# Optimization experiments

Hardware: AMD Instinct MI355X
Metric: run time of the kernel (lower is better)

Reference implementation:

```python
import jax, jax.numpy as jnp
import numpy as np

NEG_SLOPE = 0.2  # PyG GATConv default LeakyReLU slope


def gat_layer(x, src, dst, W, a_src, a_dst, bias, heads, out_dim, concat, n_nodes):
    # x: [N, F_in]; W: [F_in, heads*out_dim]
    h = (x @ W).reshape(n_nodes, heads, out_dim)          # [N, H, C]
    alpha_src = jnp.sum(h * a_src, axis=-1)               # [N, H]
    alpha_dst = jnp.sum(h * a_dst, axis=-1)               # [N, H]
    e = jax.nn.leaky_relu(alpha_src[src] + alpha_dst[dst], NEG_SLOPE)  # [E, H]
    # softmax over edges grouped by destination node (self-loops guarantee nonempty segments)
    m = jax.ops.segment_max(e, dst, num_segments=n_nodes)  # [N, H]
    w = jnp.exp(e - m[dst])
    s = jax.ops.segment_sum(w, dst, num_segments=n_nodes)  # [N, H]
    alpha = w / s[dst]                                     # [E, H]
    msg = h[src] * alpha[:, :, None]                       # [E, H, C]
    out = jax.ops.segment_sum(msg, dst, num_segments=n_nodes)  # [N, H, C]
    if concat:
        out = out.reshape(n_nodes, heads * out_dim)
    else:
        out = out.mean(axis=1)
    return out + bias


def setup_inputs() -> dict:
    key = jax.random.key(0)
    ks = jax.random.split(key, 12)
    N, E = 50000, 600000
    F_IN, OUT = 256, 64
    H1, C1 = 2, 2 * OUT          # conv1: heads=2, per-head dim 128
    F2 = H1 * C1                 # 256
    x = jax.random.normal(ks[0], (N, F_IN), dtype=jnp.float32)
    edge_index = jax.random.randint(ks[1], (2, E), 0, N, dtype=jnp.int64)
    g1 = 1.0 / np.sqrt(F_IN)
    g2 = 1.0 / np.sqrt(F2)
    return {
        "x": x,
        "edge_index": edge_index,
        "W1": jax.random.normal(ks[2], (F_IN, H1 * C1), dtype=jnp.float32) * g1,
        "a1_src": jax.random.normal(ks[3], (H1, C1), dtype=jnp.float32) * g2,
        "a1_dst": jax.random.normal(ks[4], (H1, C1), dtype=jnp.float32) * g2,
        "b1": jnp.zeros((H1 * C1,), dtype=jnp.float32),
        "W2": jax.random.normal(ks[5], (F2, OUT), dtype=jnp.float32) * g2,
        "a2_src": jax.random.normal(ks[6], (1, OUT), dtype=jnp.float32) * 0.1,
        "a2_dst": jax.random.normal(ks[7], (1, OUT), dtype=jnp.float32) * 0.1,
        "b2": jnp.zeros((OUT,), dtype=jnp.float32),
    }


def reference(x, edge_index, W1, a1_src, a1_dst, b1, W2, a2_src, a2_dst, b2):
    N = x.shape[0]
    # add self-loops (PyG GATConv default)
    loops = jnp.arange(N, dtype=edge_index.dtype)
    src = jnp.concatenate([edge_index[0], loops])
    dst = jnp.concatenate([edge_index[1], loops])
    OUT = W2.shape[1]
    h = gat_layer(x, src, dst, W1, a1_src, a1_dst, b1,
                  heads=2, out_dim=2 * OUT, concat=True, n_nodes=N)
    h = jax.nn.elu(h)
    out = gat_layer(h, src, dst, W2, a2_src, a2_dst, b2,
                    heads=1, out_dim=OUT, concat=False, n_nodes=N)
    return out
```

## Files before the change

### kernel.cpp

```cpp
#include <hip/hip_runtime.h>
#include <hip/hip_bf16.h>
#include <math.h>


#define NSLOPE 0.2f

using bf16x8 = __attribute__((ext_vector_type(8))) short;
using f32x4  = __attribute__((ext_vector_type(4))) float;
using u16x8  = __attribute__((ext_vector_type(8))) unsigned short;
using u16x4  = __attribute__((ext_vector_type(4))) unsigned short;

__device__ __forceinline__ unsigned short bf16_rne(float f) {
    unsigned u = __float_as_uint(f);
    return (unsigned short)((u + 0x7FFFu + ((u >> 16) & 1u)) >> 16);
}
__device__ __forceinline__ float bf16_to_f(unsigned short h) {
    return __uint_as_float(((unsigned)h) << 16);
}

__global__ __launch_bounds__(256) void k_prep_all(const float* __restrict__ x,
                                                  const float* __restrict__ W1,
                                                  const float* __restrict__ W2,
                                                  unsigned short* __restrict__ Xhi,
                                                  unsigned short* __restrict__ W1hi,
                                                  unsigned short* __restrict__ W2hi,
                                                  int* __restrict__ cnt,
                                                  int BX, int total4, int N) {
    int b = blockIdx.x, t = threadIdx.x;
    if (b < BX) {
        int id = b * 256 + t;
        if (id >= total4) return;
        float4 v = *(const float4*)&x[(size_t)id * 4];
        unsigned short hi[4];
        hi[0] = bf16_rne(v.x); hi[1] = bf16_rne(v.y);
        hi[2] = bf16_rne(v.z); hi[3] = bf16_rne(v.w);
        *(u16x4*)&Xhi[(size_t)id * 4] = *(u16x4*)hi;
    } else if (b < BX + 64) {
        int id = (b - BX) * 256 + t;
        int n = id >> 6, kg = id & 63;
        unsigned short hi[4];
#pragma unroll
        for (int c = 0; c < 4; ++c) {
            float w = W1[(kg * 4 + c) * 256 + n];
            hi[c] = bf16_rne(w);
        }
        *(u16x4*)&W1hi[n * 256 + kg * 4] = *(u16x4*)hi;
    } else if (b < BX + 128) {
        int id = (b - BX - 64) * 256 + t;
        int n = id >> 8, k = id & 255;
        W2hi[n * 256 + k] = bf16_rne(W2[k * 64 + n]);
    } else {
        int i = (b - BX - 128) * 256 + t;
        if (i < N) cnt[i] = 0;
    }
}

#define G1S 40
__global__ __launch_bounds__(256) void k_gemm1(const unsigned short* __restrict__ Xhi,
                                               const unsigned short* __restrict__ Whi,
                                               const float* __restrict__ a1s,
                                               const float* __restrict__ a1d,
                                               unsigned short* __restrict__ h1b,
                                               float* __restrict__ as_,
                                               float* __restrict__ ad_, int M,
                                               const int* __restrict__ esrc,
                                               const int* __restrict__ edst,
                                               int* __restrict__ cnt,
                                               int* __restrict__ bucket,
                                               int E, int G1B) {
    __shared__ unsigned short sAh[128 * G1S];
    __shared__ unsigned short sBh[256 * G1S];
    __shared__ float salS[128][2], salD[128][2];
    int t = threadIdx.x;
    if (blockIdx.x >= G1B) {
        int i = (blockIdx.x - G1B) * 256 + t;
        if (i < E) {
            int s = esrc[i], d = edst[i];
            int p = atomicAdd(&cnt[d], 1);
            if (p < 63) bucket[(size_t)d * 64 + p] = s;
        }
        return;
    }
    int lane = t & 63, wave = t >> 6;
    int q = lane >> 4, m = lane & 15;
    int row0 = blockIdx.x * 128;
    int rbase = (wave & 1) * 64;
    int head = wave >> 1;
    int cbase = head * 128;
    f32x4 acc[4][8];
#pragma unroll
    for (int i = 0; i < 4; ++i)
#pragma unroll
        for (int j = 0; j < 8; ++j) acc[i][j] = (f32x4){0.f, 0.f, 0.f, 0.f};

    for (int kc = 0; kc < 256; kc += 32) {
#pragma unroll
        for (int i2 = 0; i2 < 2; ++i2) {
            int slot = t + i2 * 256;
            int r = slot >> 2, kg = slot & 3;
            int row = row0 + r;
            u16x8 vh = {0, 0, 0, 0, 0, 0, 0, 0};
            if (row < M) vh = *(const u16x8*)&Xhi[(size_t)row * 256 + kc + kg * 8];
            *(u16x8*)&sAh[r * G1S + kg * 8] = vh;
        }
#pragma unroll
        for (int i2 = 0; i2 < 4; ++i2) {
            int slot = t + i2 * 256;
            int n = slot >> 2, kg = slot & 3;
            *(u16x8*)&sBh[n * G1S + kg * 8] =
                *(const u16x8*)&Whi[(size_t)n * 256 + kc + kg * 8];
        }
        __syncthreads();
        bf16x8 ah[4], bh[8];
#pragma unroll
        for (int i = 0; i < 4; ++i)
            ah[i] = *(bf16x8*)&sAh[(rbase + i * 16 + m) * G1S + q * 8];
#pragma unroll
        for (int j = 0; j < 8; ++j)
            bh[j] = *(bf16x8*)&sBh[(cbase + j * 16 + m) * G1S + q * 8];
#pragma unroll
        for (int i = 0; i < 4; ++i)
#pragma unroll
            for (int j = 0; j < 8; ++j)
                acc[i][j] = __builtin_amdgcn_mfma_f32_16x16x32_bf16(ah[i], bh[j], acc[i][j], 0, 0, 0);
        __syncthreads();
    }
    float sv[8], dv[8];
#pragma unroll
    for (int j = 0; j < 8; ++j) {
        sv[j] = a1s[cbase + j * 16 + m];
        dv[j] = a1d[cbase + j * 16 + m];
    }
#pragma unroll
    for (int i = 0; i < 4; ++i) {
#pragma unroll
        for (int r = 0; r < 4; ++r) {
            int rl = rbase + i * 16 + q * 4 + r;
            int row = row0 + rl;
            float ps = 0.f, pd = 0.f;
#pragma unroll
            for (int j = 0; j < 8; ++j) {
                ps += acc[i][j][r] * sv[j];
                pd += acc[i][j][r] * dv[j];
            }
#pragma unroll
            for (int mask = 1; mask < 16; mask <<= 1) {
                ps += __shfl_xor(ps, mask, 64);
                pd += __shfl_xor(pd, mask, 64);
            }
            if (m == 0) {
                salS[rl][head] = ps;
                salD[rl][head] = pd;
            }
            if (row < M) {
#pragma unroll
                for (int j = 0; j < 8; ++j)
                    h1b[(size_t)row * 256 + cbase + j * 16 + m] = bf16_rne(acc[i][j][r]);
            }
        }
    }
    __syncthreads();
    if (t < 128) {
        int row = row0 + t;
        if (row < M) {
            as_[row * 2 + 0] = salS[t][0];
            as_[row * 2 + 1] = salS[t][1];
            ad_[row * 2 + 0] = salD[t][0];
            ad_[row * 2 + 1] = salD[t][1];
        }
    }
}

__global__ __launch_bounds__(256) void k_agg1(const unsigned short* __restrict__ h1b,
                                              const float* __restrict__ as,
                                              const float* __restrict__ ad,
                                              const int* __restrict__ cnt,
                                              const int* __restrict__ bucket,
                                              const float* __restrict__ b1,
                                              unsigned short* __restrict__ helu_b, int N) {
    int wid = (blockIdx.x * blockDim.x + threadIdx.x) >> 6;
    int lane = threadIdx.x & 63;
    if (wid >= N) return;
    int c = min(cnt[wid], 63);
    int cntTot = c + 1;
    float ad0 = ad[wid * 2], ad1 = ad[wid * 2 + 1];
    int half = lane >> 5, hl = lane & 31;
    int headL = hl >> 4;
    float acc[8];
#pragma unroll
    for (int cc = 0; cc < 8; ++cc) acc[cc] = 0.f;
    float sumw = 0.f;

    int s = (lane < c) ? bucket[(size_t)wid * 64 + lane] : wid;
    float w0 = 0.f, w1 = 0.f;
    if (lane <= c) {
        float2 av = *(const float2*)&as[s * 2];
        float l0 = av.x + ad0; l0 = l0 >= 0.f ? l0 : NSLOPE * l0;
        float l1 = av.y + ad1; l1 = l1 >= 0.f ? l1 : NSLOPE * l1;
        w0 = __expf(l0); w1 = __expf(l1);
    }
    int pairs = (cntTot + 1) >> 1;
    int jj = 0;
    for (; jj + 4 <= pairs; jj += 4) {
        int e0 = 2 * jj + half, e1 = e0 + 2, e2 = e0 + 4, e3 = e0 + 6;
        int sa = __shfl(s, e0, 64), sb = __shfl(s, e1, 64);
        int sc = __shfl(s, e2, 64), se = __shfl(s, e3, 64);
        float wa0 = __shfl(w0, e0, 64), wa1 = __shfl(w1, e0, 64);
        float wb0 = __shfl(w0, e1, 64), wb1 = __shfl(w1, e1, 64);
        float wc0 = __shfl(w0, e2, 64), wc1 = __shfl(w1, e2, 64);
        float wd0 = __shfl(w0, e3, 64), wd1 = __shfl(w1, e3, 64);
        u16x8 hva = *(const u16x8*)&h1b[(size_t)sa * 256 + hl * 8];
        u16x8 hvb = *(const u16x8*)&h1b[(size_t)sb * 256 + hl * 8];
        u16x8 hvc = *(const u16x8*)&h1b[(size_t)sc * 256 + hl * 8];
        u16x8 hvd = *(const u16x8*)&h1b[(size_t)se * 256 + hl * 8];
        float wa = headL ? wa1 : wa0;
        float wb = headL ? wb1 : wb0;
        float wc = headL ? wc1 : wc0;
        float wd = headL ? wd1 : wd0;
        sumw += (wa + wb) + (wc + wd);
#pragma unroll
        for (int cc = 0; cc < 8; ++cc)
            acc[cc] += (wa * bf16_to_f(hva[cc]) + wb * bf16_to_f(hvb[cc]))
                     + (wc * bf16_to_f(hvc[cc]) + wd * bf16_to_f(hvd[cc]));
    }
    for (; jj + 2 <= pairs; jj += 2) {
        int e0 = 2 * jj + half, e1 = e0 + 2;
        int sa = __shfl(s, e0, 64), sb = __shfl(s, e1, 64);
        float wa0 = __shfl(w0, e0, 64), wa1 = __shfl(w1, e0, 64);
        float wb0 = __shfl(w0, e1, 64), wb1 = __shfl(w1, e1, 64);
        u16x8 hva = *(const u16x8*)&h1b[(size_t)sa * 256 + hl * 8];
        u16x8 hvb = *(const u16x8*)&h1b[(size_t)sb * 256 + hl * 8];
        float wa = headL ? wa1 : wa0;
        float wb = headL ? wb1 : wb0;
        sumw += wa + wb;
#pragma unroll
        for (int cc = 0; cc < 8; ++cc)
            acc[cc] += wa * bf16_to_f(hva[cc]) + wb * bf16_to_f(hvb[cc]);
    }
    for (; jj < pairs; ++jj) {
        int e0 = 2 * jj + half;
        int sa = __shfl(s, e0, 64);
        float wa0 = __shfl(w0, e0, 64), wa1 = __shfl(w1, e0, 64);
        u16x8 hva = *(const u16x8*)&h1b[(size_t)sa * 256 + hl * 8];
        float wa = headL ? wa1 : wa0;
        sumw += wa;
#pragma unroll
        for (int cc = 0; cc < 8; ++cc) acc[cc] += wa * bf16_to_f(hva[cc]);
    }
#pragma unroll
    for (int cc = 0; cc < 8; ++cc) acc[cc] += __shfl_xor(acc[cc], 32, 64);
    sumw += __shfl_xor(sumw, 32, 64);
    float inv = 1.0f / sumw;
    int ch = hl * 8 + half * 4;
    float4 bv = *(const float4*)&b1[ch];
    float bb[4] = {bv.x, bv.y, bv.z, bv.w};
    unsigned short o[4];
#pragma unroll
    for (int cc = 0; cc < 4; ++cc) {
        float v = acc[half * 4 + cc] * inv + bb[cc];
        v = v > 0.f ? v : expm1f(v);
        o[cc] = bf16_rne(v);
    }
    *(u16x4*)&helu_b[(size_t)wid * 256 + ch] = *(u16x4*)o;
}

__global__ __launch_bounds__(256) void k_gemm2(const unsigned short* __restrict__ hb,
                                               const unsigned short* __restrict__ Whi,
                                               const float* __restrict__ a2s,
                                               const float* __restrict__ a2d,
                                               unsigned short* __restrict__ h2b,
                                               float* __restrict__ as_,
                                               float* __restrict__ ad_, int M) {
    __shared__ unsigned short sA[128 * G1S];
    __shared__ unsigned short sBh[64 * G1S];
    int t = threadIdx.x;
    int lane = t & 63, wave = t >> 6;
    int q = lane >> 4, m = lane & 15;
    int row0 = blockIdx.x * 128;
    int rbase = wave * 32;
    f32x4 acc[2][4];
#pragma unroll
    for (int i = 0; i < 2; ++i)
#pragma unroll
        for (int j = 0; j < 4; ++j) acc[i][j] = (f32x4){0.f, 0.f, 0.f, 0.f};

    for (int kc = 0; kc < 256; kc += 32) {
#pragma unroll
        for (int i = 0; i < 2; ++i) {
            int slot = t + i * 256;
            int r = slot >> 2, kg = slot & 3;
            int row = row0 + r;
            u16x8 v = {0, 0, 0, 0, 0, 0, 0, 0};
            if (row < M) v = *(const u16x8*)&hb[(size_t)row * 256 + kc + kg * 8];
            *(u16x8*)&sA[r * G1S + kg * 8] = v;
        }
        {
            int n = t >> 2, kg = t & 3;
            *(u16x8*)&sBh[n * G1S + kg * 8] =
                *(const u16x8*)&Whi[(size_t)n * 256 + kc + kg * 8];
        }
        __syncthreads();
        bf16x8 a[2], bh[4];
#pragma unroll
        for (int i = 0; i < 2; ++i)
            a[i] = *(bf16x8*)&sA[(rbase + i * 16 + m) * G1S + q * 8];
#pragma unroll
        for (int j = 0; j < 4; ++j)
            bh[j] = *(bf16x8*)&sBh[(j * 16 + m) * G1S + q * 8];
#pragma unroll
        for (int i = 0; i < 2; ++i)
#pragma unroll
            for (int j = 0; j < 4; ++j)
                acc[i][j] = __builtin_amdgcn_mfma_f32_16x16x32_bf16(a[i], bh[j], acc[i][j], 0, 0, 0);
        __syncthreads();
    }
    float sv[4], dv[4];
#pragma unroll
    for (int j = 0; j < 4; ++j) {
        sv[j] = a2s[j * 16 + m];
        dv[j] = a2d[j * 16 + m];
    }
#pragma unroll
    for (int i = 0; i < 2; ++i) {
#pragma unroll
        for (int r = 0; r < 4; ++r) {
            int row = row0 + rbase + i * 16 + q * 4 + r;
            float ps = acc[i][0][r] * sv[0] + acc[i][1][r] * sv[1]
                     + acc[i][2][r] * sv[2] + acc[i][3][r] * sv[3];
            float pd = acc[i][0][r] * dv[0] + acc[i][1][r] * dv[1]
                     + acc[i][2][r] * dv[2] + acc[i][3][r] * dv[3];
#pragma unroll
            for (int mask = 1; mask < 16; mask <<= 1) {
                ps += __shfl_xor(ps, mask, 64);
                pd += __shfl_xor(pd, mask, 64);
            }
            if (row < M) {
#pragma unroll
                for (int j = 0; j < 4; ++j)
                    h2b[(size_t)row * 64 + j * 16 + m] = bf16_rne(acc[i][j][r]);
                if (m == 0) { as_[row] = ps; ad_[row] = pd; }
            }
        }
    }
}

__global__ __launch_bounds__(256) void k_agg2(const unsigned short* __restrict__ h2b,
                                              const float* __restrict__ as,
                                              const float* __restrict__ ad,
                                              const int* __restrict__ cnt,
                                              const int* __restrict__ bucket,
                                              const float* __restrict__ b2,
                                              float* __restrict__ out, int N) {
    int wid = (blockIdx.x * blockDim.x + threadIdx.x) >> 6;
    int lane = threadIdx.x & 63;
    if (wid >= N) return;
    int c = min(cnt[wid], 63);
    int cntTot = c + 1;
    float adw = ad[wid];
    int g = lane >> 4, gl = lane & 15;
    float acc[4];
#pragma unroll
    for (int cc = 0; cc < 4; ++cc) acc[cc] = 0.f;
    float sumw = 0.f;

    int s = (lane < c) ? bucket[(size_t)wid * 64 + lane] : wid;
    float w = 0.f;
    if (lane <= c) {
        float l = as[s] + adw;
        l = l >= 0.f ? l : NSLOPE * l;
        w = __expf(l);
    }
    int quads = (cntTot + 3) >> 2;
    int jj = 0;
    for (; jj + 4 <= quads; jj += 4) {
        int e0 = 4 * jj + g, e1 = e0 + 4, e2 = e0 + 8, e3 = e0 + 12;
        int sa = __shfl(s, e0, 64), sb = __shfl(s, e1, 64);
        int sc = __shfl(s, e2, 64), se = __shfl(s, e3, 64);
        float wa = __shfl(w, e0, 64), wb = __shfl(w, e1, 64);
        float wc = __shfl(w, e2, 64), wd = __shfl(w, e3, 64);
        u16x4 hva = *(const u16x4*)&h2b[(size_t)sa * 64 + gl * 4];
        u16x4 hvb = *(const u16x4*)&h2b[(size_t)sb * 64 + gl * 4];
        u16x4 hvc = *(const u16x4*)&h2b[(size_t)sc * 64 + gl * 4];
        u16x4 hvd = *(const u16x4*)&h2b[(size_t)se * 64 + gl * 4];
        sumw += (wa + wb) + (wc + wd);
        acc[0] += (wa * bf16_to_f(hva.x) + wb * bf16_to_f(hvb.x))
                + (wc * bf16_to_f(hvc.x) + wd * bf16_to_f(hvd.x));
        acc[1] += (wa * bf16_to_f(hva.y) + wb * bf16_to_f(hvb.y))
                + (wc * bf16_to_f(hvc.y) + wd * bf16_to_f(hvd.y));
        acc[2] += (wa * bf16_to_f(hva.z) + wb * bf16_to_f(hvb.z))
                + (wc * bf16_to_f(hvc.z) + wd * bf16_to_f(hvd.z));
        acc[3] += (wa * bf16_to_f(hva.w) + wb * bf16_to_f(hvb.w))
                + (wc * bf16_to_f(hvc.w) + wd * bf16_to_f(hvd.w));
    }
    for (; jj + 2 <= quads; jj += 2) {
        int e0 = 4 * jj + g, e1 = e0 + 4;
        int sa = __shfl(s, e0, 64), sb = __shfl(s, e1, 64);
        float wa = __shfl(w, e0, 64), wb = __shfl(w, e1, 64);
        u16x4 hva = *(const u16x4*)&h2b[(size_t)sa * 64 + gl * 4];
        u16x4 hvb = *(const u16x4*)&h2b[(size_t)sb * 64 + gl * 4];
        sumw += wa + wb;
        acc[0] += wa * bf16_to_f(hva.x) + wb * bf16_to_f(hvb.x);
        acc[1] += wa * bf16_to_f(hva.y) + wb * bf16_to_f(hvb.y);
        acc[2] += wa * bf16_to_f(hva.z) + wb * bf16_to_f(hvb.z);
        acc[3] += wa * bf16_to_f(hva.w) + wb * bf16_to_f(hvb.w);
    }
    for (; jj < quads; ++jj) {
        int e0 = 4 * jj + g;
        int sa = __shfl(s, e0, 64);
        float wa = __shfl(w, e0, 64);
        u16x4 hva = *(const u16x4*)&h2b[(size_t)sa * 64 + gl * 4];
        sumw += wa;
        acc[0] += wa * bf16_to_f(hva.x);
        acc[1] += wa * bf16_to_f(hva.y);
        acc[2] += wa * bf16_to_f(hva.z);
        acc[3] += wa * bf16_to_f(hva.w);
    }
#pragma unroll
    for (int cc = 0; cc < 4; ++cc) {
        acc[cc] += __shfl_xor(acc[cc], 16, 64);
        acc[cc] += __shfl_xor(acc[cc], 32, 64);
    }
    sumw += __shfl_xor(sumw, 16, 64);
    sumw += __shfl_xor(sumw, 32, 64);
    if (g == 0) {
        float inv = 1.0f / sumw;
        float4 bv = *(const float4*)&b2[gl * 4];
        float4 o;
        o.x = acc[0] * inv + bv.x;
        o.y = acc[1] * inv + bv.y;
        o.z = acc[2] * inv + bv.z;
        o.w = acc[3] * inv + bv.w;
        *(float4*)&out[(size_t)wid * 64 + gl * 4] = o;
    }
}

extern "C" void kernel_launch(void* const* d_in, const int* in_sizes, int n_in,
                              void* d_out, int out_size, void* d_ws, size_t ws_size,
                              hipStream_t stream) {
    if (n_in < 10) return;
    const float* x   = (const float*)d_in[0];
    const int*   ei  = (const int*)d_in[1];
    const float* W1  = (const float*)d_in[2];
    const float* a1s = (const float*)d_in[3];
    const float* a1d = (const float*)d_in[4];
    const float* b1  = (const float*)d_in[5];
    const float* W2  = (const float*)d_in[6];
    const float* a2s = (const float*)d_in[7];
    const float* a2d = (const float*)d_in[8];
    const float* b2  = (const float*)d_in[9];
    float* out = (float*)d_out;

    const int N = in_sizes[0] / 256;
    const int E = in_sizes[1] / 2;
    const int* esrc = ei;
    const int* edst = ei + E;

    char* ws = (char*)d_ws;
    size_t o = 0;
    auto alloc = [&](size_t bytes) -> void* {
        void* p = ws + o;
        o = (o + bytes + 255) & ~(size_t)255;
        return p;
    };
    size_t szX = (size_t)N * 256 * 2;
    char* regionA = (char*)alloc(szX);
    unsigned short* Xhi    = (unsigned short*)regionA;
    unsigned short* helu_b = (unsigned short*)regionA;

    unsigned short* h1b  = (unsigned short*)alloc((size_t)N * 256 * 2);
    unsigned short* W1hi = (unsigned short*)alloc(256 * 256 * 2);
    unsigned short* W2hi = (unsigned short*)alloc(64 * 256 * 2);
    unsigned short* h2b  = (unsigned short*)alloc((size_t)N * 64 * 2);
    float* al1s = (float*)alloc((size_t)N * 2 * 4);
    float* al1d = (float*)alloc((size_t)N * 2 * 4);
    float* al2s = (float*)alloc((size_t)N * 4);
    float* al2d = (float*)alloc((size_t)N * 4);
    int* cnt    = (int*)alloc((size_t)N * 4);
    int* bucket = (int*)alloc((size_t)N * 64 * 4);
    if (o > ws_size) return;

    const int total4 = N * 64;
    const int BX = (total4 + 255) / 256;
    const int BZ = (N + 255) / 256;
    const int G1B = (N + 127) / 128;
    const int FB = (E + 255) / 256;

    k_prep_all<<<BX + 128 + BZ, 256, 0, stream>>>(x, W1, W2, Xhi,
                                                  W1hi, W2hi, cnt,
                                                  BX, total4, N);
    k_gemm1<<<G1B + FB, 256, 0, stream>>>(Xhi, W1hi, a1s, a1d, h1b, al1s, al1d, N,
                                          esrc, edst, cnt, bucket, E, G1B);
    k_agg1<<<(N + 3) / 4, 256, 0, stream>>>(h1b, al1s, al1d, cnt, bucket, b1, helu_b, N);

    k_gemm2<<<(N + 127) / 128, 256, 0, stream>>>(helu_b, W2hi, a2s, a2d,
                                                 h2b, al2s, al2d, N);
    k_agg2<<<(N + 3) / 4, 256, 0, stream>>>(h2b, al2s, al2d, cnt, bucket, b2, out, N);
}
```

Before: 241.2 us.

## Shrink gemm1 tile to 64 rows with per-wave full-width output

Restructures the first GEMM so each block covers 64 rows instead of 128, with each wave computing a 16-row strip across all 256 output columns (both heads). This cuts accumulator registers from 128 to 64 floats per lane and shrinks the A tile in shared memory, so the kernel can declare four resident blocks per CU. Per-row attention logits for both heads are now computed within one wave and written directly, which removes the shared-memory staging and the extra barrier. In exchange the B tile is reused across fewer rows, so W is loaded from global and LDS more times in total, and twice as many blocks are launched.

```diff
diff --git a/kernel.cpp b/kernel.cpp
--- a/kernel.cpp
+++ b/kernel.cpp
@@ -56,24 +56,23 @@
 }
 
 #define G1S 40
-__global__ __launch_bounds__(256) void k_gemm1(const unsigned short* __restrict__ Xhi,
-                                               const unsigned short* __restrict__ Whi,
-                                               const float* __restrict__ a1s,
-                                               const float* __restrict__ a1d,
-                                               unsigned short* __restrict__ h1b,
-                                               float* __restrict__ as_,
-                                               float* __restrict__ ad_, int M,
-                                               const int* __restrict__ esrc,
-                                               const int* __restrict__ edst,
-                                               int* __restrict__ cnt,
-                                               int* __restrict__ bucket,
-                                               int E, int G1B) {
-    __shared__ unsigned short sAh[128 * G1S];
+__global__ __launch_bounds__(256, 4) void k_gemm1(const unsigned short* __restrict__ Xhi,
+                                                  const unsigned short* __restrict__ Whi,
+                                                  const float* __restrict__ a1s,
+                                                  const float* __restrict__ a1d,
+                                                  unsigned short* __restrict__ h1b,
+                                                  float* __restrict__ as_,
+                                                  float* __restrict__ ad_, int M,
+                                                  const int* __restrict__ esrc,
+                                                  const int* __restrict__ edst,
+                                                  int* __restrict__ cnt,
+                                                  int* __restrict__ bucket,
+                                                  int E, int NG) {
+    __shared__ unsigned short sAh[64 * G1S];
     __shared__ unsigned short sBh[256 * G1S];
-    __shared__ float salS[128][2], salD[128][2];
     int t = threadIdx.x;
-    if (blockIdx.x >= G1B) {
-        int i = (blockIdx.x - G1B) * 256 + t;
+    if (blockIdx.x >= NG) {
+        int i = (blockIdx.x - NG) * 256 + t;
         if (i < E) {
             int s = esrc[i], d = edst[i];
             int p = atomicAdd(&cnt[d], 1);
@@ -83,21 +82,15 @@
     }
     int lane = t & 63, wave = t >> 6;
     int q = lane >> 4, m = lane & 15;
-    int row0 = blockIdx.x * 128;
-    int rbase = (wave & 1) * 64;
-    int head = wave >> 1;
-    int cbase = head * 128;
-    f32x4 acc[4][8];
-#pragma unroll
-    for (int i = 0; i < 4; ++i)
-#pragma unroll
-        for (int j = 0; j < 8; ++j) acc[i][j] = (f32x4){0.f, 0.f, 0.f, 0.f};
+    int row0 = blockIdx.x * 64;
+    int rbase = wave * 16;
+    f32x4 acc[16];
+#pragma unroll
+    for (int j = 0; j < 16; ++j) acc[j] = (f32x4){0.f, 0.f, 0.f, 0.f};
 
     for (int kc = 0; kc < 256; kc += 32) {
-#pragma unroll
-        for (int i2 = 0; i2 < 2; ++i2) {
-            int slot = t + i2 * 256;
-            int r = slot >> 2, kg = slot & 3;
+        {
+            int r = t >> 2, kg = t & 3;
             int row = row0 + r;
             u16x8 vh = {0, 0, 0, 0, 0, 0, 0, 0};
             if (row < M) vh = *(const u16x8*)&Xhi[(size_t)row * 256 + kc + kg * 8];
@@ -111,62 +104,48 @@
                 *(const u16x8*)&Whi[(size_t)n * 256 + kc + kg * 8];
         }
         __syncthreads();
-        bf16x8 ah[4], bh[8];
-#pragma unroll
-        for (int i = 0; i < 4; ++i)
-            ah[i] = *(bf16x8*)&sAh[(rbase + i * 16 + m) * G1S + q * 8];
-#pragma unroll
-        for (int j = 0; j < 8; ++j)
-            bh[j] = *(bf16x8*)&sBh[(cbase + j * 16 + m) * G1S + q * 8];
-#pragma unroll
-        for (int i = 0; i < 4; ++i)
-#pragma unroll
-            for (int j = 0; j < 8; ++j)
-                acc[i][j] = __builtin_amdgcn_mfma_f32_16x16x32_bf16(ah[i], bh[j], acc[i][j], 0, 0, 0);
+        bf16x8 ah = *(bf16x8*)&sAh[(rbase + m) * G1S + q * 8];
+#pragma unroll
+        for (int j = 0; j < 16; ++j) {
+            bf16x8 bh = *(bf16x8*)&sBh[(j * 16 + m) * G1S + q * 8];
+            acc[j] = __builtin_amdgcn_mfma_f32_16x16x32_bf16(ah, bh, acc[j], 0, 0, 0);
+        }
         __syncthreads();
     }
-    float sv[8], dv[8];
-#pragma unroll
-    for (int j = 0; j < 8; ++j) {
-        sv[j] = a1s[cbase + j * 16 + m];
-        dv[j] = a1d[cbase + j * 16 + m];
-    }
-#pragma unroll
-    for (int i = 0; i < 4; ++i) {
-#pragma unroll
-        for (int r = 0; r < 4; ++r) {
-            int rl = rbase + i * 16 + q * 4 + r;
-            int row = row0 + rl;
-            float ps = 0.f, pd = 0.f;
-#pragma unroll
-            for (int j = 0; j < 8; ++j) {
-                ps += acc[i][j][r] * sv[j];
-                pd += acc[i][j][r] * dv[j];
+    float sv[16], dv[16];
+#pragma unroll
+    for (int j = 0; j < 16; ++j) {
+        sv[j] = a1s[j * 16 + m];
+        dv[j] = a1d[j * 16 + m];
+    }
+#pragma unroll
+    for (int r = 0; r < 4; ++r) {
+        int row = row0 + rbase + q * 4 + r;
+        float ps0 = 0.f, pd0 = 0.f, ps1 = 0.f, pd1 = 0.f;
+#pragma unroll
+        for (int j = 0; j < 8; ++j) {
+            ps0 += acc[j][r] * sv[j];
+            pd0 += acc[j][r] * dv[j];
+            ps1 += acc[8 + j][r] * sv[8 + j];
+            pd1 += acc[8 + j][r] * dv[8 + j];
+        }
+#pragma unroll
+        for (int mask = 1; mask < 16; mask <<= 1) {
+            ps0 += __shfl_xor(ps0, mask, 64);
+            pd0 += __shfl_xor(pd0, mask, 64);
+            ps1 += __shfl_xor(ps1, mask, 64);
+            pd1 += __shfl_xor(pd1, mask, 64);
+        }
+        if (row < M) {
+#pragma unroll
+            for (int j = 0; j < 16; ++j)
+                h1b[(size_t)row * 256 + j * 16 + m] = bf16_rne(acc[j][r]);
+            if (m == 0) {
+                as_[row * 2 + 0] = ps0;
+                as_[row * 2 + 1] = ps1;
+                ad_[row * 2 + 0] = pd0;
+                ad_[row * 2 + 1] = pd1;
             }
-#pragma unroll
-            for (int mask = 1; mask < 16; mask <<= 1) {
-                ps += __shfl_xor(ps, mask, 64);
-                pd += __shfl_xor(pd, mask, 64);
-            }
-            if (m == 0) {
-                salS[rl][head] = ps;
-                salD[rl][head] = pd;
-            }
-            if (row < M) {
-#pragma unroll
-                for (int j = 0; j < 8; ++j)
-                    h1b[(size_t)row * 256 + cbase + j * 16 + m] = bf16_rne(acc[i][j][r]);
-            }
-        }
-    }
-    __syncthreads();
-    if (t < 128) {
-        int row = row0 + t;
-        if (row < M) {
-            as_[row * 2 + 0] = salS[t][0];
-            as_[row * 2 + 1] = salS[t][1];
-            ad_[row * 2 + 0] = salD[t][0];
-            ad_[row * 2 + 1] = salD[t][1];
         }
     }
 }
@@ -482,14 +461,14 @@
     const int total4 = N * 64;
     const int BX = (total4 + 255) / 256;
     const int BZ = (N + 255) / 256;
-    const int G1B = (N + 127) / 128;
+    const int NG = (N + 63) / 64;
     const int FB = (E + 255) / 256;
 
     k_prep_all<<<BX + 128 + BZ, 256, 0, stream>>>(x, W1, W2, Xhi,
                                                   W1hi, W2hi, cnt,
                                                   BX, total4, N);
-    k_gemm1<<<G1B + FB, 256, 0, stream>>>(Xhi, W1hi, a1s, a1d, h1b, al1s, al1d, N,
-                                          esrc, edst, cnt, bucket, E, G1B);
+    k_gemm1<<<NG + FB, 256, 0, stream>>>(Xhi, W1hi, a1s, a1d, h1b, al1s, al1d, N,
+                                         esrc, edst, cnt, bucket, E, NG);
     k_agg1<<<(N + 3) / 4, 256, 0, stream>>>(h1b, al1s, al1d, cnt, bucket, b1, helu_b, N);
 
     k_gemm2<<<(N + 127) / 128, 256, 0, stream>>>(helu_b, W2hi, a2s, a2d,
```

Measured after the change: 241.1 us. No clear change (-0.0%).
